# Performance work log

Hardware: AMD Instinct MI355X
Metric: run time of the kernel (lower is better)

## Reference

```python
import jax, jax.numpy as jnp
import numpy as np

N_NODES = 50000
N_EDGES = 800000
IN_FEATS = 96
HIDDEN = 48


def setup_inputs() -> dict:
    key = jax.random.key(0)
    ks = jax.random.split(key, 16)
    x = jax.random.normal(ks[0], (N_NODES, IN_FEATS), dtype=jnp.float32)
    edge_index = jax.random.randint(ks[1], (2, N_EDGES), 0, N_NODES, dtype=jnp.int32)

    def lin(k, fan_in, fan_out):
        s = 1.0 / np.sqrt(fan_in)
        return jax.random.uniform(k, (fan_in, fan_out), jnp.float32, -s, s)

    return {
        "x": x,
        "edge_index": edge_index,
        # SAGEConv layer 0: in -> hidden
        "w_self0": lin(ks[2], IN_FEATS, HIDDEN),
        "w_neigh0": lin(ks[3], IN_FEATS, HIDDEN),
        "b0": jnp.zeros((HIDDEN,), jnp.float32),
        # SAGEConv layer 1: hidden -> hidden
        "w_self1": lin(ks[4], HIDDEN, HIDDEN),
        "w_neigh1": lin(ks[5], HIDDEN, HIDDEN),
        "b1": jnp.zeros((HIDDEN,), jnp.float32),
        # SAGEConv layer 2: hidden -> hidden
        "w_self2": lin(ks[6], HIDDEN, HIDDEN),
        "w_neigh2": lin(ks[7], HIDDEN, HIDDEN),
        "b2": jnp.zeros((HIDDEN,), jnp.float32),
        # prediction head: hidden -> 1
        "w_pred": lin(ks[8], HIDDEN, 1),
        "b_pred": jnp.zeros((1,), jnp.float32),
    }


def _sage_mean(x, src, dst, deg_inv, w_self, w_neigh, b):
    # mean over in-neighbors: gather src features, segment-sum at dst, / in-degree
    agg = jax.ops.segment_sum(x[src], dst, num_segments=N_NODES) * deg_inv  # [N, F]
    return x @ w_self + agg @ w_neigh + b


def reference(x, edge_index, w_self0, w_neigh0, b0, w_self1, w_neigh1, b1,
              w_self2, w_neigh2, b2, w_pred, b_pred):
    src, dst = edge_index[0], edge_index[1]
    deg = jax.ops.segment_sum(jnp.ones((src.shape[0],), x.dtype), dst,
                              num_segments=N_NODES)
    deg_inv = (1.0 / jnp.maximum(deg, 1.0))[:, None]  # isolated nodes -> 0 agg

    h = jax.nn.relu(_sage_mean(x, src, dst, deg_inv, w_self0, w_neigh0, b0))
    h = jax.nn.relu(_sage_mean(h, src, dst, deg_inv, w_self1, w_neigh1, b1))
    h = jax.nn.relu(_sage_mean(h, src, dst, deg_inv, w_self2, w_neigh2, b2))
    return h @ w_pred + b_pred  # [N, 1]
```

## Files before the change

kernel.cpp:

```cpp
#include <hip/hip_runtime.h>
#include <hip/hip_fp16.h>


constexpr int HID = 48;
constexpr int MAXDEG = 64;
constexpr int GNB = 64;

__device__ __forceinline__ unsigned pack_h2(float a, float b) {
    __half2 h = __floats2half2_rn(a, b);
    return *reinterpret_cast<unsigned*>(&h);
}
__device__ __forceinline__ void acc_u2(float* g, uint2 u) {
    __half2 h0 = *reinterpret_cast<__half2*>(&u.x);
    __half2 h1 = *reinterpret_cast<__half2*>(&u.y);
    float2 f0 = __half22float2(h0), f1 = __half22float2(h1);
    g[0] += f0.x; g[1] += f0.y; g[2] += f1.x; g[3] += f1.y;
}
__device__ __forceinline__ void unpack_u2(float* v, uint2 u) {
    __half2 h0 = *reinterpret_cast<__half2*>(&u.x);
    __half2 h1 = *reinterpret_cast<__half2*>(&u.y);
    float2 f0 = __half22float2(h0), f1 = __half22float2(h1);
    v[0] = f0.x; v[1] = f0.y; v[2] = f1.x; v[3] = f1.y;
}
__device__ __forceinline__ void fma12_h(const uint2* __restrict__ wrow, float s,
                                        float* acc) {
    uint2 w0 = wrow[0], w1 = wrow[1], w2 = wrow[2];
    float v[12];
    unpack_u2(v + 0, w0); unpack_u2(v + 4, w1); unpack_u2(v + 8, w2);
#pragma unroll
    for (int j = 0; j < 12; ++j) acc[j] = fmaf(s, v[j], acc[j]);
}

__device__ __forceinline__ void gather_h4(const __half* __restrict__ p,
                                          const unsigned short* __restrict__ bkt,
                                          int deg, int e, int jb, float* g) {
    float ga[12], gb[12];
#pragma unroll
    for (int j = 0; j < 12; ++j) { ga[j] = 0.0f; gb[j] = 0.0f; }
    int i = e;
    for (; i + 6 < deg; i += 8) {
        int s0 = bkt[i], s1 = bkt[i + 2], s2 = bkt[i + 4], s3 = bkt[i + 6];
        const uint2* r0 = reinterpret_cast<const uint2*>(p + (size_t)s0 * HID + jb);
        const uint2* r1 = reinterpret_cast<const uint2*>(p + (size_t)s1 * HID + jb);
        const uint2* r2 = reinterpret_cast<const uint2*>(p + (size_t)s2 * HID + jb);
        const uint2* r3 = reinterpret_cast<const uint2*>(p + (size_t)s3 * HID + jb);
        uint2 a0 = r0[0], a1 = r0[1], a2 = r0[2];
        uint2 b0 = r1[0], b1 = r1[1], b2 = r1[2];
        uint2 c0 = r2[0], c1 = r2[1], c2 = r2[2];
        uint2 d0 = r3[0], d1 = r3[1], d2 = r3[2];
        acc_u2(ga + 0, a0); acc_u2(ga + 4, a1); acc_u2(ga + 8, a2);
        acc_u2(gb + 0, b0); acc_u2(gb + 4, b1); acc_u2(gb + 8, b2);
        acc_u2(ga + 0, c0); acc_u2(ga + 4, c1); acc_u2(ga + 8, c2);
        acc_u2(gb + 0, d0); acc_u2(gb + 4, d1); acc_u2(gb + 8, d2);
    }
    for (; i + 2 < deg; i += 4) {
        int s0 = bkt[i], s1 = bkt[i + 2];
        const uint2* r0 = reinterpret_cast<const uint2*>(p + (size_t)s0 * HID + jb);
        const uint2* r1 = reinterpret_cast<const uint2*>(p + (size_t)s1 * HID + jb);
        uint2 a0 = r0[0], a1 = r0[1], a2 = r0[2];
        uint2 b0 = r1[0], b1 = r1[1], b2 = r1[2];
        acc_u2(ga + 0, a0); acc_u2(ga + 4, a1); acc_u2(ga + 8, a2);
        acc_u2(gb + 0, b0); acc_u2(gb + 4, b1); acc_u2(gb + 8, b2);
    }
    if (i < deg) {
        const uint2* r0 = reinterpret_cast<const uint2*>(p + (size_t)bkt[i] * HID + jb);
        uint2 a0 = r0[0], a1 = r0[1], a2 = r0[2];
        acc_u2(ga + 0, a0); acc_u2(ga + 4, a1); acc_u2(ga + 8, a2);
    }
#pragma unroll
    for (int j = 0; j < 12; ++j) g[j] = ga[j] + gb[j];
#pragma unroll
    for (int j = 0; j < 12; ++j) g[j] += __shfl_xor(g[j], 4, 64);
}

__global__ __launch_bounds__(128) void fill_proj_k(
    const float* __restrict__ X, const float* __restrict__ Wn,
    const float* __restrict__ Ws, const float* __restrict__ bias,
    __half* __restrict__ p_out, float* __restrict__ s_out, int n_nodes,
    const int* __restrict__ src, const int* __restrict__ dst,
    int* __restrict__ cnt, unsigned short* __restrict__ buckets,
    int n_edges, int gemm_blocks) {
    __shared__ float wlds[96 * HID];
    __shared__ float bias_lds[HID];
    const int t = threadIdx.x;

    if ((int)blockIdx.x >= gemm_blocks) {
        int base = (blockIdx.x - gemm_blocks) * 256 + t;
        int e0 = base, e1 = base + 128;
        if (e0 < n_edges) {
            int d = dst[e0];
            int s = src[e0];
            int pos = atomicAdd(&cnt[d], 1);
            if (pos < MAXDEG) buckets[(size_t)d * MAXDEG + pos] = (unsigned short)s;
        }
        if (e1 < n_edges) {
            int d = dst[e1];
            int s = src[e1];
            int pos = atomicAdd(&cnt[d], 1);
            if (pos < MAXDEG) buckets[(size_t)d * MAXDEG + pos] = (unsigned short)s;
        }
        return;
    }

    const int q = t & 3;
    const int m = t >> 2;
    const int jb = q * 12;
    const int n0 = blockIdx.x * GNB + 2 * m;
    const int n1 = n0 + 1;
    const bool v0 = n0 < n_nodes, v1 = n1 < n_nodes;
    const int cn0 = v0 ? n0 : 0, cn1 = v1 ? n1 : 0;
    const float4* xr0 = reinterpret_cast<const float4*>(X + (size_t)cn0 * 96);
    const float4* xr1 = reinterpret_cast<const float4*>(X + (size_t)cn1 * 96);

    for (int i = t; i < 96 * HID; i += 128) wlds[i] = Wn[i];
    __syncthreads();
    {
        float pa[12], pb[12];
#pragma unroll
        for (int j = 0; j < 12; ++j) { pa[j] = 0.0f; pb[j] = 0.0f; }
#pragma unroll 4
        for (int k4 = 0; k4 < 24; ++k4) {
            float4 xa = xr0[k4];
            float4 xb = xr1[k4];
#pragma unroll
            for (int c = 0; c < 4; ++c) {
                float x0 = (c == 0) ? xa.x : (c == 1) ? xa.y : (c == 2) ? xa.z : xa.w;
                float x1 = (c == 0) ? xb.x : (c == 1) ? xb.y : (c == 2) ? xb.z : xb.w;
                const float4* wr =
                    reinterpret_cast<const float4*>(&wlds[(k4 * 4 + c) * HID + jb]);
#pragma unroll
                for (int j4 = 0; j4 < 3; ++j4) {
                    float4 wv = wr[j4];
                    pa[j4 * 4 + 0] = fmaf(x0, wv.x, pa[j4 * 4 + 0]);
                    pa[j4 * 4 + 1] = fmaf(x0, wv.y, pa[j4 * 4 + 1]);
                    pa[j4 * 4 + 2] = fmaf(x0, wv.z, pa[j4 * 4 + 2]);
                    pa[j4 * 4 + 3] = fmaf(x0, wv.w, pa[j4 * 4 + 3]);
                    pb[j4 * 4 + 0] = fmaf(x1, wv.x, pb[j4 * 4 + 0]);
                    pb[j4 * 4 + 1] = fmaf(x1, wv.y, pb[j4 * 4 + 1]);
                    pb[j4 * 4 + 2] = fmaf(x1, wv.z, pb[j4 * 4 + 2]);
                    pb[j4 * 4 + 3] = fmaf(x1, wv.w, pb[j4 * 4 + 3]);
                }
            }
        }
        if (v0) {
            uint2* po = reinterpret_cast<uint2*>(p_out + (size_t)n0 * HID + jb);
            po[0] = make_uint2(pack_h2(pa[0], pa[1]), pack_h2(pa[2], pa[3]));
            po[1] = make_uint2(pack_h2(pa[4], pa[5]), pack_h2(pa[6], pa[7]));
            po[2] = make_uint2(pack_h2(pa[8], pa[9]), pack_h2(pa[10], pa[11]));
        }
        if (v1) {
            uint2* po = reinterpret_cast<uint2*>(p_out + (size_t)n1 * HID + jb);
            po[0] = make_uint2(pack_h2(pb[0], pb[1]), pack_h2(pb[2], pb[3]));
            po[1] = make_uint2(pack_h2(pb[4], pb[5]), pack_h2(pb[6], pb[7]));
            po[2] = make_uint2(pack_h2(pb[8], pb[9]), pack_h2(pb[10], pb[11]));
        }
    }
    __syncthreads();

    for (int i = t; i < 96 * HID; i += 128) wlds[i] = Ws[i];
    if (t < HID) bias_lds[t] = bias[t];
    __syncthreads();
    {
        float sa[12], sb[12];
#pragma unroll
        for (int j = 0; j < 12; ++j) {
            float b = bias_lds[jb + j];
            sa[j] = b; sb[j] = b;
        }
#pragma unroll 4
        for (int k4 = 0; k4 < 24; ++k4) {
            float4 xa = xr0[k4];
            float4 xb = xr1[k4];
#pragma unroll
            for (int c = 0; c < 4; ++c) {
                float x0 = (c == 0) ? xa.x : (c == 1) ? xa.y : (c == 2) ? xa.z : xa.w;
                float x1 = (c == 0) ? xb.x : (c == 1) ? xb.y : (c == 2) ? xb.z : xb.w;
                const float4* wr =
                    reinterpret_cast<const float4*>(&wlds[(k4 * 4 + c) * HID + jb]);
#pragma unroll
                for (int j4 = 0; j4 < 3; ++j4) {
                    float4 wv = wr[j4];
                    sa[j4 * 4 + 0] = fmaf(x0, wv.x, sa[j4 * 4 + 0]);
                    sa[j4 * 4 + 1] = fmaf(x0, wv.y, sa[j4 * 4 + 1]);
                    sa[j4 * 4 + 2] = fmaf(x0, wv.z, sa[j4 * 4 + 2]);
                    sa[j4 * 4 + 3] = fmaf(x0, wv.w, sa[j4 * 4 + 3]);
                    sb[j4 * 4 + 0] = fmaf(x1, wv.x, sb[j4 * 4 + 0]);
                    sb[j4 * 4 + 1] = fmaf(x1, wv.y, sb[j4 * 4 + 1]);
                    sb[j4 * 4 + 2] = fmaf(x1, wv.z, sb[j4 * 4 + 2]);
                    sb[j4 * 4 + 3] = fmaf(x1, wv.w, sb[j4 * 4 + 3]);
                }
            }
        }
        float4* so0 = reinterpret_cast<float4*>(s_out + (size_t)cn0 * HID + jb);
        float4* so1 = reinterpret_cast<float4*>(s_out + (size_t)cn1 * HID + jb);
#pragma unroll
        for (int j4 = 0; j4 < 3; ++j4) {
            if (v0) so0[j4] = make_float4(sa[j4 * 4 + 0], sa[j4 * 4 + 1],
                                          sa[j4 * 4 + 2], sa[j4 * 4 + 3]);
            if (v1) so1[j4] = make_float4(sb[j4 * 4 + 0], sb[j4 * 4 + 1],
                                          sb[j4 * 4 + 2], sb[j4 * 4 + 3]);
        }
    }
}

__global__ __launch_bounds__(128, 6) void act_k(
    const __half* __restrict__ p_in, const float* __restrict__ s_in,
    const int* __restrict__ cnt, const unsigned short* __restrict__ buckets,
    __half* __restrict__ h_out, int n_nodes) {
    const int t = threadIdx.x;
    const int q = t & 3;
    const int e = (t >> 2) & 1;
    const int m = t >> 3;
    const int n = blockIdx.x * 16 + m;
    if (n >= n_nodes) return;
    const int jb = q * 12;

    const int deg = min(cnt[n], MAXDEG);
    const float di = 1.0f / fmaxf((float)deg, 1.0f);
    float g[12];
    gather_h4(p_in, buckets + (size_t)n * MAXDEG, deg, e, jb, g);

    if (e == 0) {
        const float4* sr = reinterpret_cast<const float4*>(s_in + (size_t)n * HID + jb);
        float h[12];
#pragma unroll
        for (int j4 = 0; j4 < 3; ++j4) {
            float4 sv = sr[j4];
            h[j4 * 4 + 0] = fmaxf(fmaf(di, g[j4 * 4 + 0], sv.x), 0.0f);
            h[j4 * 4 + 1] = fmaxf(fmaf(di, g[j4 * 4 + 1], sv.y), 0.0f);
            h[j4 * 4 + 2] = fmaxf(fmaf(di, g[j4 * 4 + 2], sv.z), 0.0f);
            h[j4 * 4 + 3] = fmaxf(fmaf(di, g[j4 * 4 + 3], sv.w), 0.0f);
        }
        uint2* ho = reinterpret_cast<uint2*>(h_out + (size_t)n * HID + jb);
        ho[0] = make_uint2(pack_h2(h[0], h[1]), pack_h2(h[2], h[3]));
        ho[1] = make_uint2(pack_h2(h[4], h[5]), pack_h2(h[6], h[7]));
        ho[2] = make_uint2(pack_h2(h[8], h[9]), pack_h2(h[10], h[11]));
    }
}

template <bool LAST>
__global__ __launch_bounds__(128, 6) void layer_k(
    const __half* __restrict__ h_in, const int* __restrict__ cnt,
    const unsigned short* __restrict__ buckets, const float* __restrict__ wn,
    const float* __restrict__ ws, const float* __restrict__ bn,
    const float* __restrict__ w_pred, const float* __restrict__ b_pred,
    __half* __restrict__ h_out, float* __restrict__ out, int n_nodes) {
    __shared__ uint2 wn_s[HID * HID / 4];
    __shared__ uint2 ws_s[HID * HID / 4];
    __shared__ float bn_lds[HID];
    __shared__ float wp_lds[HID];

    const int t = threadIdx.x;
    for (int i4 = t; i4 < HID * HID / 4; i4 += 128) {
        float4 a = reinterpret_cast<const float4*>(wn)[i4];
        float4 b = reinterpret_cast<const float4*>(ws)[i4];
        wn_s[i4] = make_uint2(pack_h2(a.x, a.y), pack_h2(a.z, a.w));
        ws_s[i4] = make_uint2(pack_h2(b.x, b.y), pack_h2(b.z, b.w));
    }
    if (t < HID) bn_lds[t] = bn[t];
    if (LAST && t < HID) wp_lds[t] = w_pred[t];
    __syncthreads();

    const int q = t & 3;
    const int e = (t >> 2) & 1;
    const int m = t >> 3;
    const int n = blockIdx.x * 16 + m;
    if (n >= n_nodes) return;
    const int jb = q * 12;

    const int deg = min(cnt[n], MAXDEG);
    const float di = 1.0f / fmaxf((float)deg, 1.0f);
    float g[12];
    gather_h4(h_in, buckets + (size_t)n * MAXDEG, deg, e, jb, g);
#pragma unroll
    for (int j = 0; j < 12; ++j) g[j] *= di;

    float hs_own[12];
    {
        const uint2* hr = reinterpret_cast<const uint2*>(h_in + (size_t)n * HID + jb);
        uint2 a = hr[0], b = hr[1], c = hr[2];
        unpack_u2(hs_own + 0, a); unpack_u2(hs_own + 4, b); unpack_u2(hs_own + 8, c);
    }

    float acc[12];
#pragma unroll
    for (int j = 0; j < 12; ++j) acc[j] = (e == 0) ? bn_lds[jb + j] : 0.0f;

    const int kb = e * 24;
#pragma unroll
    for (int kk = 0; kk < 24; ++kk) {
        const int k = kb + kk;
        const int srcl = (t & ~3) | (k / 12);
        float gs = __shfl(g[kk % 12], srcl, 64);
        float hv = __shfl(hs_own[kk % 12], srcl, 64);
        fma12_h(&wn_s[(k * HID + jb) >> 2], gs, acc);
        fma12_h(&ws_s[(k * HID + jb) >> 2], hv, acc);
    }
#pragma unroll
    for (int j = 0; j < 12; ++j) acc[j] += __shfl_xor(acc[j], 4, 64);

    if (LAST) {
        float s = 0.0f;
#pragma unroll
        for (int j = 0; j < 12; ++j) s = fmaf(fmaxf(acc[j], 0.0f), wp_lds[jb + j], s);
        s += __shfl_xor(s, 1, 64);
        s += __shfl_xor(s, 2, 64);
        if ((t & 7) == 0) out[n] = s + b_pred[0];
        return;
    }

    if (e == 0) {
        float h[12];
#pragma unroll
        for (int j = 0; j < 12; ++j) h[j] = fmaxf(acc[j], 0.0f);
        uint2* ho = reinterpret_cast<uint2*>(h_out + (size_t)n * HID + jb);
        ho[0] = make_uint2(pack_h2(h[0], h[1]), pack_h2(h[2], h[3]));
        ho[1] = make_uint2(pack_h2(h[4], h[5]), pack_h2(h[6], h[7]));
        ho[2] = make_uint2(pack_h2(h[8], h[9]), pack_h2(h[10], h[11]));
    }
}

extern "C" void kernel_launch(void* const* d_in, const int* in_sizes, int n_in,
                              void* d_out, int out_size, void* d_ws, size_t ws_size,
                              hipStream_t stream) {
    const float* x        = (const float*)d_in[0];
    const int*   ei       = (const int*)d_in[1];
    const float* w_self0  = (const float*)d_in[2];
    const float* w_neigh0 = (const float*)d_in[3];
    const float* b0       = (const float*)d_in[4];
    const float* w_self1  = (const float*)d_in[5];
    const float* w_neigh1 = (const float*)d_in[6];
    const float* b1       = (const float*)d_in[7];
    const float* w_self2  = (const float*)d_in[8];
    const float* w_neigh2 = (const float*)d_in[9];
    const float* b2       = (const float*)d_in[10];
    const float* w_pred   = (const float*)d_in[11];
    const float* b_pred   = (const float*)d_in[12];

    const int n_nodes = in_sizes[0] / 96;
    const int n_edges = in_sizes[1] / 2;
    const int* src = ei;
    const int* dst = ei + n_edges;

    char* wsb = (char*)d_ws;
    int* cnt                = (int*)wsb;              wsb += (size_t)n_nodes * 4;
    unsigned short* buckets = (unsigned short*)wsb;   wsb += (size_t)n_nodes * MAXDEG * 2;
    __half* p0 = (__half*)wsb;                        wsb += (size_t)n_nodes * HID * 2;
    __half* h1 = (__half*)wsb;                        wsb += (size_t)n_nodes * HID * 2;
    __half* h2 = (__half*)wsb;                        wsb += (size_t)n_nodes * HID * 2;
    float* s0 = (float*)wsb;                          wsb += (size_t)n_nodes * HID * 4;
    float* out = (float*)d_out;

    const int gnb = (n_nodes + GNB - 1) / GNB;
    const int fb = (n_edges + 255) / 256;
    const int lb = (n_nodes + 15) / 16;

    hipMemsetAsync(cnt, 0, (size_t)n_nodes * 4, stream);

    fill_proj_k<<<gnb + fb, 128, 0, stream>>>(x, w_neigh0, w_self0, b0, p0, s0,
                                              n_nodes, src, dst, cnt, buckets,
                                              n_edges, gnb);
    act_k<<<lb, 128, 0, stream>>>(p0, s0, cnt, buckets, h1, n_nodes);
    layer_k<false><<<lb, 128, 0, stream>>>(h1, cnt, buckets, w_neigh1, w_self1,
                                           b1, nullptr, nullptr, h2, nullptr,
                                           n_nodes);
    layer_k<true><<<lb, 128, 0, stream>>>(h2, cnt, buckets, w_neigh2, w_self2,
                                          b2, w_pred, b_pred, nullptr, out,
                                          n_nodes);
}
```

Baseline: 209.0 us.

## Sort nodes by degree for load balance and fuse fp16 dual-weight projection

```diff
diff --git a/kernel.cpp b/kernel.cpp
--- a/kernel.cpp
+++ b/kernel.cpp
@@ -80,7 +80,8 @@
     const int* __restrict__ src, const int* __restrict__ dst,
     int* __restrict__ cnt, unsigned short* __restrict__ buckets,
     int n_edges, int gemm_blocks) {
-    __shared__ float wlds[96 * HID];
+    __shared__ uint2 wn_s[96 * HID / 4];
+    __shared__ uint2 ws_s[96 * HID / 4];
     __shared__ float bias_lds[HID];
     const int t = threadIdx.x;
 
@@ -102,9 +103,19 @@
         return;
     }
 
+    for (int i4 = t; i4 < 96 * HID / 4; i4 += 128) {
+        float4 a = reinterpret_cast<const float4*>(Wn)[i4];
+        float4 b = reinterpret_cast<const float4*>(Ws)[i4];
+        wn_s[i4] = make_uint2(pack_h2(a.x, a.y), pack_h2(a.z, a.w));
+        ws_s[i4] = make_uint2(pack_h2(b.x, b.y), pack_h2(b.z, b.w));
+    }
+    if (t < HID) bias_lds[t] = bias[t];
+    __syncthreads();
+
     const int q = t & 3;
     const int m = t >> 2;
     const int jb = q * 12;
+    const int q3 = q * 3;
     const int n0 = blockIdx.x * GNB + 2 * m;
     const int n1 = n0 + 1;
     const bool v0 = n0 < n_nodes, v1 = n1 < n_nodes;
@@ -112,107 +123,102 @@
     const float4* xr0 = reinterpret_cast<const float4*>(X + (size_t)cn0 * 96);
     const float4* xr1 = reinterpret_cast<const float4*>(X + (size_t)cn1 * 96);
 
-    for (int i = t; i < 96 * HID; i += 128) wlds[i] = Wn[i];
-    __syncthreads();
-    {
-        float pa[12], pb[12];
-#pragma unroll
-        for (int j = 0; j < 12; ++j) { pa[j] = 0.0f; pb[j] = 0.0f; }
-#pragma unroll 4
-        for (int k4 = 0; k4 < 24; ++k4) {
-            float4 xa = xr0[k4];
-            float4 xb = xr1[k4];
-#pragma unroll
-            for (int c = 0; c < 4; ++c) {
-                float x0 = (c == 0) ? xa.x : (c == 1) ? xa.y : (c == 2) ? xa.z : xa.w;
-                float x1 = (c == 0) ? xb.x : (c == 1) ? xb.y : (c == 2) ? xb.z : xb.w;
-                const float4* wr =
-                    reinterpret_cast<const float4*>(&wlds[(k4 * 4 + c) * HID + jb]);
-#pragma unroll
-                for (int j4 = 0; j4 < 3; ++j4) {
-                    float4 wv = wr[j4];
-                    pa[j4 * 4 + 0] = fmaf(x0, wv.x, pa[j4 * 4 + 0]);
-                    pa[j4 * 4 + 1] = fmaf(x0, wv.y, pa[j4 * 4 + 1]);
-                    pa[j4 * 4 + 2] = fmaf(x0, wv.z, pa[j4 * 4 + 2]);
-                    pa[j4 * 4 + 3] = fmaf(x0, wv.w, pa[j4 * 4 + 3]);
-                    pb[j4 * 4 + 0] = fmaf(x1, wv.x, pb[j4 * 4 + 0]);
-                    pb[j4 * 4 + 1] = fmaf(x1, wv.y, pb[j4 * 4 + 1]);
-                    pb[j4 * 4 + 2] = fmaf(x1, wv.z, pb[j4 * 4 + 2]);
-                    pb[j4 * 4 + 3] = fmaf(x1, wv.w, pb[j4 * 4 + 3]);
-                }
+    float pa[12], pb[12], sa[12], sb[12];
+#pragma unroll
+    for (int j = 0; j < 12; ++j) {
+        pa[j] = 0.0f; pb[j] = 0.0f;
+        float b = bias_lds[jb + j];
+        sa[j] = b; sb[j] = b;
+    }
+#pragma unroll 2
+    for (int k4 = 0; k4 < 24; ++k4) {
+        float4 xa = xr0[k4];
+        float4 xb = xr1[k4];
+#pragma unroll
+        for (int c = 0; c < 4; ++c) {
+            const int k = k4 * 4 + c;
+            float x0 = (c == 0) ? xa.x : (c == 1) ? xa.y : (c == 2) ? xa.z : xa.w;
+            float x1 = (c == 0) ? xb.x : (c == 1) ? xb.y : (c == 2) ? xb.z : xb.w;
+            const uint2* wr = &wn_s[k * 12 + q3];
+            const uint2* ur = &ws_s[k * 12 + q3];
+            float vn[12], vs[12];
+            uint2 w0 = wr[0], w1 = wr[1], w2 = wr[2];
+            uint2 u0 = ur[0], u1 = ur[1], u2 = ur[2];
+            unpack_u2(vn + 0, w0); unpack_u2(vn + 4, w1); unpack_u2(vn + 8, w2);
+            unpack_u2(vs + 0, u0); unpack_u2(vs + 4, u1); unpack_u2(vs + 8, u2);
+#pragma unroll
+            for (int j = 0; j < 12; ++j) {
+                pa[j] = fmaf(x0, vn[j], pa[j]);
+                pb[j] = fmaf(x1, vn[j], pb[j]);
+                sa[j] = fmaf(x0, vs[j], sa[j]);
+                sb[j] = fmaf(x1, vs[j], sb[j]);
             }
         }
-        if (v0) {
-            uint2* po = reinterpret_cast<uint2*>(p_out + (size_t)n0 * HID + jb);
-            po[0] = make_uint2(pack_h2(pa[0], pa[1]), pack_h2(pa[2], pa[3]));
-            po[1] = make_uint2(pack_h2(pa[4], pa[5]), pack_h2(pa[6], pa[7]));
-            po[2] = make_uint2(pack_h2(pa[8], pa[9]), pack_h2(pa[10], pa[11]));
-        }
-        if (v1) {
-            uint2* po = reinterpret_cast<uint2*>(p_out + (size_t)n1 * HID + jb);
-            po[0] = make_uint2(pack_h2(pb[0], pb[1]), pack_h2(pb[2], pb[3]));
-            po[1] = make_uint2(pack_h2(pb[4], pb[5]), pack_h2(pb[6], pb[7]));
-            po[2] = make_uint2(pack_h2(pb[8], pb[9]), pack_h2(pb[10], pb[11]));
-        }
-    }
-    __syncthreads();
-
-    for (int i = t; i < 96 * HID; i += 128) wlds[i] = Ws[i];
-    if (t < HID) bias_lds[t] = bias[t];
-    __syncthreads();
-    {
-        float sa[12], sb[12];
-#pragma unroll
-        for (int j = 0; j < 12; ++j) {
-            float b = bias_lds[jb + j];
-            sa[j] = b; sb[j] = b;
-        }
-#pragma unroll 4
-        for (int k4 = 0; k4 < 24; ++k4) {
-            float4 xa = xr0[k4];
-            float4 xb = xr1[k4];
-#pragma unroll
-            for (int c = 0; c < 4; ++c) {
-                float x0 = (c == 0) ? xa.x : (c == 1) ? xa.y : (c == 2) ? xa.z : xa.w;
-                float x1 = (c == 0) ? xb.x : (c == 1) ? xb.y : (c == 2) ? xb.z : xb.w;
-                const float4* wr =
-                    reinterpret_cast<const float4*>(&wlds[(k4 * 4 + c) * HID + jb]);
-#pragma unroll
-                for (int j4 = 0; j4 < 3; ++j4) {
-                    float4 wv = wr[j4];
-                    sa[j4 * 4 + 0] = fmaf(x0, wv.x, sa[j4 * 4 + 0]);
-                    sa[j4 * 4 + 1] = fmaf(x0, wv.y, sa[j4 * 4 + 1]);
-                    sa[j4 * 4 + 2] = fmaf(x0, wv.z, sa[j4 * 4 + 2]);
-                    sa[j4 * 4 + 3] = fmaf(x0, wv.w, sa[j4 * 4 + 3]);
-                    sb[j4 * 4 + 0] = fmaf(x1, wv.x, sb[j4 * 4 + 0]);
-                    sb[j4 * 4 + 1] = fmaf(x1, wv.y, sb[j4 * 4 + 1]);
-                    sb[j4 * 4 + 2] = fmaf(x1, wv.z, sb[j4 * 4 + 2]);
-                    sb[j4 * 4 + 3] = fmaf(x1, wv.w, sb[j4 * 4 + 3]);
-                }
-            }
-        }
-        float4* so0 = reinterpret_cast<float4*>(s_out + (size_t)cn0 * HID + jb);
-        float4* so1 = reinterpret_cast<float4*>(s_out + (size_t)cn1 * HID + jb);
-#pragma unroll
-        for (int j4 = 0; j4 < 3; ++j4) {
-            if (v0) so0[j4] = make_float4(sa[j4 * 4 + 0], sa[j4 * 4 + 1],
-                                          sa[j4 * 4 + 2], sa[j4 * 4 + 3]);
-            if (v1) so1[j4] = make_float4(sb[j4 * 4 + 0], sb[j4 * 4 + 1],
-                                          sb[j4 * 4 + 2], sb[j4 * 4 + 3]);
-        }
+    }
+    if (v0) {
+        uint2* po = reinterpret_cast<uint2*>(p_out + (size_t)n0 * HID + jb);
+        po[0] = make_uint2(pack_h2(pa[0], pa[1]), pack_h2(pa[2], pa[3]));
+        po[1] = make_uint2(pack_h2(pa[4], pa[5]), pack_h2(pa[6], pa[7]));
+        po[2] = make_uint2(pack_h2(pa[8], pa[9]), pack_h2(pa[10], pa[11]));
+        float4* so = reinterpret_cast<float4*>(s_out + (size_t)n0 * HID + jb);
+        so[0] = make_float4(sa[0], sa[1], sa[2], sa[3]);
+        so[1] = make_float4(sa[4], sa[5], sa[6], sa[7]);
+        so[2] = make_float4(sa[8], sa[9], sa[10], sa[11]);
+    }
+    if (v1) {
+        uint2* po = reinterpret_cast<uint2*>(p_out + (size_t)n1 * HID + jb);
+        po[0] = make_uint2(pack_h2(pb[0], pb[1]), pack_h2(pb[2], pb[3]));
+        po[1] = make_uint2(pack_h2(pb[4], pb[5]), pack_h2(pb[6], pb[7]));
+        po[2] = make_uint2(pack_h2(pb[8], pb[9]), pack_h2(pb[10], pb[11]));
+        float4* so = reinterpret_cast<float4*>(s_out + (size_t)n1 * HID + jb);
+        so[0] = make_float4(sb[0], sb[1], sb[2], sb[3]);
+        so[1] = make_float4(sb[4], sb[5], sb[6], sb[7]);
+        so[2] = make_float4(sb[8], sb[9], sb[10], sb[11]);
+    }
+}
+
+__global__ __launch_bounds__(256) void hist_k(const int* __restrict__ cnt,
+                                              int* __restrict__ hist, int n) {
+    int i = blockIdx.x * 256 + threadIdx.x;
+    if (i < n) {
+        int b = min(min(cnt[i], MAXDEG), 63);
+        atomicAdd(&hist[b], 1);
+    }
+}
+__global__ __launch_bounds__(64) void scan_k(const int* __restrict__ hist,
+                                             int* __restrict__ binoff) {
+    int t = threadIdx.x;
+    int v = hist[t];
+    int incl = v;
+    for (int off = 1; off < 64; off <<= 1) {
+        int u = __shfl_up(incl, off, 64);
+        if (t >= off) incl += u;
+    }
+    binoff[t] = incl - v;
+}
+__global__ __launch_bounds__(256) void perm_k(const int* __restrict__ cnt,
+                                              const int* __restrict__ binoff,
+                                              int* __restrict__ cursor,
+                                              int* __restrict__ perm, int n) {
+    int i = blockIdx.x * 256 + threadIdx.x;
+    if (i < n) {
+        int b = min(min(cnt[i], MAXDEG), 63);
+        int pos = atomicAdd(&cursor[b], 1);
+        perm[binoff[b] + pos] = i;
     }
 }
 
 __global__ __launch_bounds__(128, 6) void act_k(
     const __half* __restrict__ p_in, const float* __restrict__ s_in,
     const int* __restrict__ cnt, const unsigned short* __restrict__ buckets,
-    __half* __restrict__ h_out, int n_nodes) {
+    const int* __restrict__ perm, __half* __restrict__ h_out, int n_nodes) {
     const int t = threadIdx.x;
     const int q = t & 3;
     const int e = (t >> 2) & 1;
     const int m = t >> 3;
-    const int n = blockIdx.x * 16 + m;
-    if (n >= n_nodes) return;
+    const int idx = blockIdx.x * 16 + m;
+    if (idx >= n_nodes) return;
+    const int n = perm[idx];
     const int jb = q * 12;
 
     const int deg = min(cnt[n], MAXDEG);
@@ -241,10 +247,11 @@
 template <bool LAST>
 __global__ __launch_bounds__(128, 6) void layer_k(
     const __half* __restrict__ h_in, const int* __restrict__ cnt,
-    const unsigned short* __restrict__ buckets, const float* __restrict__ wn,
-    const float* __restrict__ ws, const float* __restrict__ bn,
-    const float* __restrict__ w_pred, const float* __restrict__ b_pred,
-    __half* __restrict__ h_out, float* __restrict__ out, int n_nodes) {
+    const unsigned short* __restrict__ buckets, const int* __restrict__ perm,
+    const float* __restrict__ wn, const float* __restrict__ ws,
+    const float* __restrict__ bn, const float* __restrict__ w_pred,
+    const float* __restrict__ b_pred, __half* __restrict__ h_out,
+    float* __restrict__ out, int n_nodes) {
     __shared__ uint2 wn_s[HID * HID / 4];
     __shared__ uint2 ws_s[HID * HID / 4];
     __shared__ float bn_lds[HID];
@@ -264,8 +271,9 @@
     const int q = t & 3;
     const int e = (t >> 2) & 1;
     const int m = t >> 3;
-    const int n = blockIdx.x * 16 + m;
-    if (n >= n_nodes) return;
+    const int idx = blockIdx.x * 16 + m;
+    if (idx >= n_nodes) return;
+    const int n = perm[idx];
     const int jb = q * 12;
 
     const int deg = min(cnt[n], MAXDEG);
@@ -344,6 +352,10 @@
 
     char* wsb = (char*)d_ws;
     int* cnt                = (int*)wsb;              wsb += (size_t)n_nodes * 4;
+    int* hist               = (int*)wsb;              wsb += 64 * 4;
+    int* cursor             = (int*)wsb;              wsb += 64 * 4;
+    int* binoff             = (int*)wsb;              wsb += 64 * 4;
+    int* perm               = (int*)wsb;              wsb += (size_t)n_nodes * 4;
     unsigned short* buckets = (unsigned short*)wsb;   wsb += (size_t)n_nodes * MAXDEG * 2;
     __half* p0 = (__half*)wsb;                        wsb += (size_t)n_nodes * HID * 2;
     __half* h1 = (__half*)wsb;                        wsb += (size_t)n_nodes * HID * 2;
@@ -354,17 +366,22 @@
     const int gnb = (n_nodes + GNB - 1) / GNB;
     const int fb = (n_edges + 255) / 256;
     const int lb = (n_nodes + 15) / 16;
-
-    hipMemsetAsync(cnt, 0, (size_t)n_nodes * 4, stream);
+    const int nb = (n_nodes + 255) / 256;
+
+    hipMemsetAsync(cnt, 0, ((size_t)n_nodes + 128) * 4, stream);
 
     fill_proj_k<<<gnb + fb, 128, 0, stream>>>(x, w_neigh0, w_self0, b0, p0, s0,
                                               n_nodes, src, dst, cnt, buckets,
                                               n_edges, gnb);
-    act_k<<<lb, 128, 0, stream>>>(p0, s0, cnt, buckets, h1, n_nodes);
-    layer_k<false><<<lb, 128, 0, stream>>>(h1, cnt, buckets, w_neigh1, w_self1,
-                                           b1, nullptr, nullptr, h2, nullptr,
-                                           n_nodes);
-    layer_k<true><<<lb, 128, 0, stream>>>(h2, cnt, buckets, w_neigh2, w_self2,
-                                          b2, w_pred, b_pred, nullptr, out,
-                                          n_nodes);
-}
+    hist_k<<<nb, 256, 0, stream>>>(cnt, hist, n_nodes);
+    scan_k<<<1, 64, 0, stream>>>(hist, binoff);
+    perm_k<<<nb, 256, 0, stream>>>(cnt, binoff, cursor, perm, n_nodes);
+
+    act_k<<<lb, 128, 0, stream>>>(p0, s0, cnt, buckets, perm, h1, n_nodes);
+    layer_k<false><<<lb, 128, 0, stream>>>(h1, cnt, buckets, perm, w_neigh1,
+                                           w_self1, b1, nullptr, nullptr, h2,
+                                           nullptr, n_nodes);
+    layer_k<true><<<lb, 128, 0, stream>>>(h2, cnt, buckets, perm, w_neigh2,
+                                          w_self2, b2, w_pred, b_pred, nullptr,
+                                          out, n_nodes);
+}
```

Measured after the change: 428.1 us. 2.05x slower.
